# Kernel tuning notes

Hardware: AMD Instinct MI355X
Metric: run time of the kernel (lower is better)

Reference implementation:

```python
import jax, jax.numpy as jnp
import numpy as np

BETA = 0.9  # leaky-integrator decay of the stateful neuron


def setup_inputs() -> dict:
    key = jax.random.key(0)
    k = jax.random.split(key, 5)
    B, T, I, H, O = 128, 512, 1024, 2048, 512
    x = jax.random.normal(k[0], (B, T, I), dtype=jnp.float32)
    # Linear params, PyTorch-style scaling
    W_in = jax.random.normal(k[1], (I, H), dtype=jnp.float32) / np.sqrt(I)
    b_in = jax.random.normal(k[2], (H,), dtype=jnp.float32) / np.sqrt(I)
    W_out = jax.random.normal(k[3], (H, O), dtype=jnp.float32) / np.sqrt(H)
    b_out = jax.random.normal(k[4], (O,), dtype=jnp.float32) / np.sqrt(H)
    return {"x": x, "W_in": W_in, "b_in": b_in, "W_out": W_out, "b_out": b_out}


def reference(x, W_in, b_in, W_out, b_out):
    # x: [B, T, I]
    B, T, _ = x.shape
    # fc_in applied to every timestep at once (same math as per-step Linear)
    h = jnp.einsum('bti,ih->bth', x, W_in) + b_in  # [B, T, H]

    # stateful neuron: leaky integration s_t = BETA * s_{t-1} + h_t, via scan
    def step(s, h_t):
        s = BETA * s + h_t
        return s, s

    s0 = jnp.zeros((B, h.shape[-1]), dtype=h.dtype)
    _, S = jax.lax.scan(step, s0, jnp.swapaxes(h, 0, 1))  # S: [T, B, H]

    # readout per timestep, then reduce over time (readout_mode='sum')
    logits = jnp.einsum('tbh,ho->tbo', S, W_out) + b_out  # [T, B, O]
    return logits.sum(axis=0)  # [B, O]
```

## Files before the change

### kernel.cpp

```cpp
#include <hip/hip_runtime.h>
#include <hip/hip_bf16.h>
#include <math.h>

constexpr int B_ = 128, T_ = 512, I_ = 1024, H_ = 2048, O_ = 512;
#define BETA 0.9f

constexpr int SLAB = B_ * I_;
constexpr int NSLABS = 4;
constexpr int ZOFF = NSLABS * SLAB;
constexpr int WS_FLOATS = ZOFF + B_ * H_;

typedef __attribute__((ext_vector_type(4))) short short4v;
typedef __attribute__((ext_vector_type(8))) short short8v;
typedef __attribute__((ext_vector_type(4))) float float4v;

__global__ __launch_bounds__(256) void init_kernel(float* __restrict__ ws,
                                                   const float* __restrict__ b_in,
                                                   const float* __restrict__ b_out,
                                                   float* __restrict__ out, float wsum) {
    int idx = blockIdx.x * 256 + threadIdx.x;
    const int total = B_ * H_ + B_ * O_;
    if (idx >= total) return;
    if (idx < B_ * H_) {
        ws[ZOFF + idx] = wsum * b_in[idx & (H_ - 1)];
    } else {
        int j = idx - B_ * H_;
        out[j] = (float)T_ * b_out[j & (O_ - 1)];
    }
}

constexpr int TCH = 128;
__global__ __launch_bounds__(256) void wreduce_kernel(const float* __restrict__ x,
                                                      float* __restrict__ ws) {
    __shared__ float wl[TCH];
    const int b  = blockIdx.x >> 2;
    const int tc = blockIdx.x & 3;
    const int t0 = tc * TCH;
    if (threadIdx.x < TCH)
        wl[threadIdx.x] = (1.f - powf(BETA, (float)(T_ - (t0 + threadIdx.x)))) * 10.f;
    __syncthreads();

    const int i = threadIdx.x * 4;
    const float* xp = x + (size_t)b * T_ * I_ + (size_t)t0 * I_ + i;
    float4v acc = {0.f, 0.f, 0.f, 0.f};
#pragma unroll 4
    for (int tb = 0; tb < TCH; tb += 8) {
        float4v v[8];
#pragma unroll
        for (int j = 0; j < 8; ++j)
            v[j] = *(const float4v*)(xp + (size_t)(tb + j) * I_);
#pragma unroll
        for (int j = 0; j < 8; ++j) {
            const float wt = wl[tb + j];
            acc.x += wt * v[j].x; acc.y += wt * v[j].y;
            acc.z += wt * v[j].z; acc.w += wt * v[j].w;
        }
    }
    __builtin_nontemporal_store(acc, (float4v*)(ws + (size_t)tc * SLAB + b * I_ + i));
}

template <int KGLOB, int NGLOB, int KCH, int NSL>
__global__ __launch_bounds__(256) void mm128(const float* __restrict__ A,
                                             const float* __restrict__ Bm,
                                             float* __restrict__ C) {
    constexpr int BN = 64, BK = 32, PAD = 8;
    __shared__ __align__(16) __hip_bfloat16 As[128][BK + PAD];
    __shared__ __align__(16) __hip_bfloat16 Bs[BN][BK + PAD];

    const int n0    = blockIdx.x * BN;
    const int kbase = blockIdx.y * KCH;
    const int tid   = threadIdx.x;
    const int lane  = tid & 63;
    const int w     = tid >> 6;
    const int lo    = lane & 15;
    const int hi    = lane >> 4;

    float4v acc[2][4];
#pragma unroll
    for (int mf = 0; mf < 2; ++mf)
#pragma unroll
        for (int nf = 0; nf < 4; ++nf) acc[mf][nf] = (float4v){0.f, 0.f, 0.f, 0.f};

    for (int k0 = kbase; k0 < kbase + KCH; k0 += BK) {
        {
            const int row = tid >> 1;
            const int kh  = (tid & 1) * 16;
            const float* ap = A + (size_t)row * KGLOB + k0 + kh;
#pragma unroll
            for (int j = 0; j < 4; ++j) {
                float4v v = *(const float4v*)(ap + 4 * j);
                if constexpr (NSL > 1) {
#pragma unroll
                    for (int p = 1; p < NSL; ++p)
                        v += *(const float4v*)(ap + (size_t)p * B_ * KGLOB + 4 * j);
                }
                union { short4v s; __hip_bfloat16 h[4]; } u;
                u.h[0] = __float2bfloat16(v.x); u.h[1] = __float2bfloat16(v.y);
                u.h[2] = __float2bfloat16(v.z); u.h[3] = __float2bfloat16(v.w);
                *(short4v*)&As[row][kh + 4 * j] = u.s;
            }
        }
        {
            const int k  = tid >> 3;
            const int nq = (tid & 7) * 8;
            const float* bp = Bm + (size_t)(k0 + k) * NGLOB + n0 + nq;
#pragma unroll
            for (int j = 0; j < 2; ++j) {
                float4 v = *(const float4*)(bp + 4 * j);
                Bs[nq + 4 * j + 0][k] = __float2bfloat16(v.x);
                Bs[nq + 4 * j + 1][k] = __float2bfloat16(v.y);
                Bs[nq + 4 * j + 2][k] = __float2bfloat16(v.z);
                Bs[nq + 4 * j + 3][k] = __float2bfloat16(v.w);
            }
        }
        __syncthreads();
        {
            const int kk = hi * 8;
            short8v a[2], bv[4];
#pragma unroll
            for (int mf = 0; mf < 2; ++mf)
                a[mf] = *(const short8v*)&As[w * 32 + mf * 16 + lo][kk];
#pragma unroll
            for (int nf = 0; nf < 4; ++nf)
                bv[nf] = *(const short8v*)&Bs[nf * 16 + lo][kk];
#pragma unroll
            for (int mf = 0; mf < 2; ++mf)
#pragma unroll
                for (int nf = 0; nf < 4; ++nf)
                    acc[mf][nf] = __builtin_amdgcn_mfma_f32_16x16x32_bf16(
                        a[mf], bv[nf], acc[mf][nf], 0, 0, 0);
        }
        __syncthreads();
    }
#pragma unroll
    for (int mf = 0; mf < 2; ++mf)
#pragma unroll
        for (int nf = 0; nf < 4; ++nf)
#pragma unroll
            for (int i = 0; i < 4; ++i) {
                const int row = w * 32 + mf * 16 + hi * 4 + i;
                const int col = n0 + nf * 16 + lo;
                atomicAdd(&C[(size_t)row * NGLOB + col], acc[mf][nf][i]);
            }
}

extern "C" void kernel_launch(void* const* d_in, const int* in_sizes, int n_in,
                              void* d_out, int out_size, void* d_ws, size_t ws_size,
                              hipStream_t stream) {
    const float* x     = (const float*)d_in[0];
    const float* W_in  = (const float*)d_in[1];
    const float* b_in  = (const float*)d_in[2];
    const float* W_out = (const float*)d_in[3];
    const float* b_out = (const float*)d_in[4];
    float* out = (float*)d_out;
    float* ws  = (float*)d_ws;

    const double beta = 0.9;
    const double bT = pow(beta, (double)T_);
    const float wsum = (float)(((double)T_ - beta * (1.0 - bT) / (1.0 - beta)) / (1.0 - beta));

    const int total = B_ * H_ + B_ * O_;
    init_kernel<<<(total + 255) / 256, 256, 0, stream>>>(ws, b_in, b_out, out, wsum);

    wreduce_kernel<<<B_ * (T_ / TCH), 256, 0, stream>>>(x, ws);

    mm128<I_, H_, 128, NSLABS><<<dim3(H_ / 64, I_ / 128), 256, 0, stream>>>(ws, W_in, ws + ZOFF);

    mm128<H_, O_, 64, 1><<<dim3(O_ / 64, H_ / 64), 256, 0, stream>>>(ws + ZOFF, W_out, out);
}
```

Baseline: 77.12 us.

## Fuse all stages into one cooperative kernel with grid-wide syncs

```diff
diff --git a/kernel.cpp b/kernel.cpp
--- a/kernel.cpp
+++ b/kernel.cpp
@@ -1,74 +1,34 @@
 #include <hip/hip_runtime.h>
-#include <hip/hip_bf16.h>
+#include <hip/hip_cooperative_groups.h>
 #include <math.h>
 
+namespace cg = cooperative_groups;
+
 constexpr int B_ = 128, T_ = 512, I_ = 1024, H_ = 2048, O_ = 512;
-#define BETA 0.9f
 
-constexpr int SLAB = B_ * I_;
-constexpr int NSLABS = 4;
-constexpr int ZOFF = NSLABS * SLAB;
-constexpr int WS_FLOATS = ZOFF + B_ * H_;
+constexpr int YOFF = 0;
+constexpr int ZOFF = B_ * I_;
 
 typedef __attribute__((ext_vector_type(4))) short short4v;
 typedef __attribute__((ext_vector_type(8))) short short8v;
 typedef __attribute__((ext_vector_type(4))) float float4v;
 
-__global__ __launch_bounds__(256) void init_kernel(float* __restrict__ ws,
-                                                   const float* __restrict__ b_in,
-                                                   const float* __restrict__ b_out,
-                                                   float* __restrict__ out, float wsum) {
-    int idx = blockIdx.x * 256 + threadIdx.x;
-    const int total = B_ * H_ + B_ * O_;
-    if (idx >= total) return;
-    if (idx < B_ * H_) {
-        ws[ZOFF + idx] = wsum * b_in[idx & (H_ - 1)];
-    } else {
-        int j = idx - B_ * H_;
-        out[j] = (float)T_ * b_out[j & (O_ - 1)];
-    }
+__device__ inline ushort f2bf(float f) {
+    union { float f; unsigned u; } c; c.f = f;
+    return (ushort)((c.u + 0x7FFF + ((c.u >> 16) & 1)) >> 16);
 }
 
-constexpr int TCH = 128;
-__global__ __launch_bounds__(256) void wreduce_kernel(const float* __restrict__ x,
-                                                      float* __restrict__ ws) {
-    __shared__ float wl[TCH];
-    const int b  = blockIdx.x >> 2;
-    const int tc = blockIdx.x & 3;
-    const int t0 = tc * TCH;
-    if (threadIdx.x < TCH)
-        wl[threadIdx.x] = (1.f - powf(BETA, (float)(T_ - (t0 + threadIdx.x)))) * 10.f;
-    __syncthreads();
+template <int KGLOB, int NGLOB, int KCH>
+__device__ inline void mm_body(char* smraw, int nb, int kb,
+                               const float* __restrict__ A,
+                               const float* __restrict__ Bm,
+                               float* __restrict__ C) {
+    constexpr int BN = 64, BK = 32, PAD = 8;
+    ushort (*As)[BK + PAD] = (ushort (*)[BK + PAD])smraw;
+    ushort (*Bs)[BK + PAD] = (ushort (*)[BK + PAD])(smraw + 128 * (BK + PAD) * 2);
 
-    const int i = threadIdx.x * 4;
-    const float* xp = x + (size_t)b * T_ * I_ + (size_t)t0 * I_ + i;
-    float4v acc = {0.f, 0.f, 0.f, 0.f};
-#pragma unroll 4
-    for (int tb = 0; tb < TCH; tb += 8) {
-        float4v v[8];
-#pragma unroll
-        for (int j = 0; j < 8; ++j)
-            v[j] = *(const float4v*)(xp + (size_t)(tb + j) * I_);
-#pragma unroll
-        for (int j = 0; j < 8; ++j) {
-            const float wt = wl[tb + j];
-            acc.x += wt * v[j].x; acc.y += wt * v[j].y;
-            acc.z += wt * v[j].z; acc.w += wt * v[j].w;
-        }
-    }
-    __builtin_nontemporal_store(acc, (float4v*)(ws + (size_t)tc * SLAB + b * I_ + i));
-}
-
-template <int KGLOB, int NGLOB, int KCH, int NSL>
-__global__ __launch_bounds__(256) void mm128(const float* __restrict__ A,
-                                             const float* __restrict__ Bm,
-                                             float* __restrict__ C) {
-    constexpr int BN = 64, BK = 32, PAD = 8;
-    __shared__ __align__(16) __hip_bfloat16 As[128][BK + PAD];
-    __shared__ __align__(16) __hip_bfloat16 Bs[BN][BK + PAD];
-
-    const int n0    = blockIdx.x * BN;
-    const int kbase = blockIdx.y * KCH;
+    const int n0    = nb * BN;
+    const int kbase = kb * KCH;
     const int tid   = threadIdx.x;
     const int lane  = tid & 63;
     const int w     = tid >> 6;
@@ -89,15 +49,10 @@
 #pragma unroll
             for (int j = 0; j < 4; ++j) {
                 float4v v = *(const float4v*)(ap + 4 * j);
-                if constexpr (NSL > 1) {
-#pragma unroll
-                    for (int p = 1; p < NSL; ++p)
-                        v += *(const float4v*)(ap + (size_t)p * B_ * KGLOB + 4 * j);
-                }
-                union { short4v s; __hip_bfloat16 h[4]; } u;
-                u.h[0] = __float2bfloat16(v.x); u.h[1] = __float2bfloat16(v.y);
-                u.h[2] = __float2bfloat16(v.z); u.h[3] = __float2bfloat16(v.w);
-                *(short4v*)&As[row][kh + 4 * j] = u.s;
+                short4v s;
+                s[0] = (short)f2bf(v.x); s[1] = (short)f2bf(v.y);
+                s[2] = (short)f2bf(v.z); s[3] = (short)f2bf(v.w);
+                *(short4v*)&As[row][kh + 4 * j] = s;
             }
         }
         {
@@ -106,11 +61,11 @@
             const float* bp = Bm + (size_t)(k0 + k) * NGLOB + n0 + nq;
 #pragma unroll
             for (int j = 0; j < 2; ++j) {
-                float4 v = *(const float4*)(bp + 4 * j);
-                Bs[nq + 4 * j + 0][k] = __float2bfloat16(v.x);
-                Bs[nq + 4 * j + 1][k] = __float2bfloat16(v.y);
-                Bs[nq + 4 * j + 2][k] = __float2bfloat16(v.z);
-                Bs[nq + 4 * j + 3][k] = __float2bfloat16(v.w);
+                float4v v = *(const float4v*)(bp + 4 * j);
+                Bs[nq + 4 * j + 0][k] = f2bf(v.x);
+                Bs[nq + 4 * j + 1][k] = f2bf(v.y);
+                Bs[nq + 4 * j + 2][k] = f2bf(v.z);
+                Bs[nq + 4 * j + 3][k] = f2bf(v.w);
             }
         }
         __syncthreads();
@@ -144,6 +99,68 @@
             }
 }
 
+__global__ __launch_bounds__(256, 2) void coop(const float* __restrict__ x,
+                                               const float* __restrict__ Wi,
+                                               const float* __restrict__ b_in,
+                                               const float* __restrict__ Wo,
+                                               const float* __restrict__ b_out,
+                                               float* __restrict__ ws,
+                                               float* __restrict__ out, float wsum) {
+    __shared__ __align__(16) char sm[(128 * 40 + 64 * 40) * 2];
+    const int bid = blockIdx.x, tid = threadIdx.x;
+
+    {
+        float* wl = (float*)sm;
+        float4v* red = (float4v*)(sm + 2048);
+        wl[tid]       = (1.f - powf(0.9f, (float)(T_ - tid))) * 10.f;
+        wl[tid + 256] = (1.f - powf(0.9f, (float)(T_ - (tid + 256)))) * 10.f;
+#pragma unroll
+        for (int k = tid; k < 512; k += 256) {
+            const int f = bid * 512 + k;
+            ws[ZOFF + f] = wsum * b_in[f & (H_ - 1)];
+        }
+        if (bid < 128) {
+#pragma unroll
+            for (int k = tid; k < 512; k += 256) {
+                const int f = bid * 512 + k;
+                out[f] = (float)T_ * b_out[f & (O_ - 1)];
+            }
+        }
+        __syncthreads();
+
+        const int b = bid >> 2, q = bid & 3;
+        const int lane = tid & 63, grp = tid >> 6;
+        const float* xp = x + (size_t)b * T_ * I_ + (size_t)grp * I_ + q * 256 + lane * 4;
+        float4v acc = {0.f, 0.f, 0.f, 0.f};
+#pragma unroll 2
+        for (int s8 = 0; s8 < 128; s8 += 8) {
+            float4v v[8];
+#pragma unroll
+            for (int u = 0; u < 8; ++u)
+                v[u] = *(const float4v*)(xp + (size_t)(s8 + u) * 4 * I_);
+#pragma unroll
+            for (int u = 0; u < 8; ++u)
+                acc += wl[(s8 + u) * 4 + grp] * v[u];
+        }
+        red[tid] = acc;
+        __syncthreads();
+        if (tid < 64) {
+            float4v r = red[tid] + red[tid + 64] + red[tid + 128] + red[tid + 192];
+            *(float4v*)(ws + YOFF + (size_t)b * I_ + q * 256 + tid * 4) = r;
+        }
+    }
+
+    cg::this_grid().sync();
+
+    if (bid < 256)
+        mm_body<I_, H_, 128>(sm, bid & 31, bid >> 5, ws + YOFF, Wi, ws + ZOFF);
+
+    cg::this_grid().sync();
+
+    if (bid < 256)
+        mm_body<H_, O_, 64>(sm, bid & 7, bid >> 3, ws + ZOFF, Wo, out);
+}
+
 extern "C" void kernel_launch(void* const* d_in, const int* in_sizes, int n_in,
                               void* d_out, int out_size, void* d_ws, size_t ws_size,
                               hipStream_t stream) {
@@ -159,12 +176,7 @@
     const double bT = pow(beta, (double)T_);
     const float wsum = (float)(((double)T_ - beta * (1.0 - bT) / (1.0 - beta)) / (1.0 - beta));
 
-    const int total = B_ * H_ + B_ * O_;
-    init_kernel<<<(total + 255) / 256, 256, 0, stream>>>(ws, b_in, b_out, out, wsum);
-
-    wreduce_kernel<<<B_ * (T_ / TCH), 256, 0, stream>>>(x, ws);
-
-    mm128<I_, H_, 128, NSLABS><<<dim3(H_ / 64, I_ / 128), 256, 0, stream>>>(ws, W_in, ws + ZOFF);
-
-    mm128<H_, O_, 64, 1><<<dim3(O_ / 64, H_ / 64), 256, 0, stream>>>(ws + ZOFF, W_out, out);
+    void* args[] = {(void*)&x, (void*)&W_in, (void*)&b_in, (void*)&W_out,
+                    (void*)&b_out, (void*)&ws, (void*)&out, (void*)&wsum};
+    hipLaunchCooperativeKernel((const void*)coop, dim3(512), dim3(256), args, 0, stream);
 }
```

Result: slower. 190.7 us (+147.2%).
